# Optimization experiments

Measured on AMD Instinct MI355X. Metric: run time of the kernel, lower is better.

The kernel has to match this reference:

```python
import jax, jax.numpy as jnp
import numpy as np

INF = 100000.0
B, W, T, U, S, N = 64, 16, 64, 128, 20, 8


def setup_inputs() -> dict:
    key = jax.random.key(0)
    ks = jax.random.split(key, 9)
    xavier = (2.0 / (U + U)) ** 0.5
    return {
        "slot_utt_h": jax.random.normal(ks[0], (B, W, T, U), jnp.float32),
        "slot_candidate_c": jax.random.normal(ks[1], (S, U), jnp.float32),
        "status_candidate_c": jax.random.normal(ks[2], (N, U), jnp.float32),
        "position_encoding": jax.random.normal(ks[3], (B, W, S, U), jnp.float32),
        "q_status": jax.random.normal(ks[4], (B, W, N, U), jnp.float32),
        "mask": jnp.zeros((B, W, S * N), jnp.float32),
        "weight": jax.random.normal(ks[5], (U, U), jnp.float32) * xavier,  # bilinear co-attention weight [U,U]
        "W1": jax.random.normal(ks[6], (2 * U, U), jnp.float32) * 0.05,
        "b1": jnp.zeros((U,), jnp.float32),
        "W2": jax.random.normal(ks[7], (U, U), jnp.float32) * 0.05,
        "b2": jnp.zeros((U,), jnp.float32),
        "W3": jax.random.normal(ks[8], (U, 1), jnp.float32) * 0.05,
        "b3": jnp.zeros((1,), jnp.float32),
    }


def _zero_mask(p):
    # original: -(p == 0).float() * INF, added before softmax
    return jnp.where(p == 0.0, -INF, 0.0)


def reference(slot_utt_h, slot_candidate_c, status_candidate_c, position_encoding,
              q_status, mask, weight, W1, b1, W2, b2, W3, b3):
    # ---- attention over utterance tokens ----
    # p[b,w,s,t] = <slot_candidate_c[s], slot_utt_h[b,w,t]>
    p = jnp.einsum('su,bwtu->bwst', slot_candidate_c, slot_utt_h)
    p = jax.nn.softmax(p + _zero_mask(p), axis=-1)
    q_slot = jnp.einsum('bwst,bwtu->bwsu', p, slot_utt_h) + position_encoding  # [B,W,S,U]

    # ---- bilinear co-attention: [B,W*S,U] @ weight @ [B,U,W*N] -> [B,W,S,W,N] ----
    co = jnp.einsum('bwsu,uv,bxnv->bwsxn', q_slot, weight, q_status)
    p2 = jax.nn.softmax(co + _zero_mask(co), axis=3)  # softmax over the second window axis x

    # weighted sum of statuses over window axis x
    q_status_slot = jnp.einsum('bwsxn,bxnu->bwsnu', p2, q_status)  # [B,W,S,N,U]

    q_slot_exp = jnp.broadcast_to(q_slot[:, :, :, None, :], (B, W, S, N, U))
    features = jnp.concatenate([q_slot_exp, q_status_slot], axis=-1)  # [B,W,S,N,2U]

    # ---- MLP (dropout in eval mode = identity) ----
    h = jax.nn.relu(features @ W1 + b1)
    h = jax.nn.relu(h @ W2 + b2)
    logits = h @ W3 + b3  # [B,W,S,N,1]

    logits = logits.reshape(B, W, S * N)
    slot_pred_logits = jnp.max(logits + mask, axis=1)  # masked max-pool over window
    slot_pred_labels = (slot_pred_logits > 0.0).astype(jnp.float32)
    return (slot_pred_labels, S * N, slot_pred_logits)
```

## Files before the change

kernel.cpp:

```cpp
#include <hip/hip_runtime.h>
#include <math.h>

#define INF_ 100000.0f
constexpr int B_ = 64, W_ = 16, T_ = 64, U_ = 128, S_ = 20, N_ = 8;

typedef unsigned short ushort_t;
typedef __attribute__((ext_vector_type(8))) short bf16x8;
typedef __attribute__((ext_vector_type(4))) float floatx4;

static __device__ __forceinline__ unsigned short f2bf(float x) {
    unsigned int u = __float_as_uint(x);
    return (unsigned short)((u + 0x7fff + ((u >> 16) & 1)) >> 16);
}
static __device__ __forceinline__ float bf2f(unsigned short s) {
    return __uint_as_float(((unsigned int)s) << 16);
}

#define HT_SWZ(u, t) ((u) * 72 + ((t) ^ ((((u) >> 3) & 7) << 3)))

__global__ __launch_bounds__(256) void k_pre(
    const float* __restrict__ q_status, const float* __restrict__ weight,
    const float* __restrict__ W1, const float* __restrict__ W2,
    const float* __restrict__ c,
    ushort_t* __restrict__ w1topT, ushort_t* __restrict__ w2T,
    ushort_t* __restrict__ c_bf,
    ushort_t* __restrict__ Gt_bf, ushort_t* __restrict__ qs1T_bf)
{
    __shared__ __align__(16) ushort_t sw[128 * 136];
    __shared__ __align__(16) ushort_t sq[128 * 136];
    const int tid = threadIdx.x, bx = blockIdx.x;

    if (bx < 64) {
        const int b = bx;
        const float* qb = q_status + (size_t)b * 16384;
        for (int i = tid * 4; i < 16384; i += 1024) {
            int r = i >> 7, v = i & 127;
            float4 wv = *(const float4*)&weight[i];
            *(ushort4*)&sw[r * 136 + v] =
                (ushort4){f2bf(wv.x), f2bf(wv.y), f2bf(wv.z), f2bf(wv.w)};
            float4 qv = *(const float4*)&qb[i];
            *(ushort4*)&sq[r * 136 + v] =
                (ushort4){f2bf(qv.x), f2bf(qv.y), f2bf(qv.z), f2bf(qv.w)};
        }
        __syncthreads();
        const int wave = tid >> 6, lane = tid & 63, m16 = lane & 15, q = lane >> 4;
        ushort_t* Gb = Gt_bf + (size_t)b * 16384;
#pragma unroll
        for (int ci = 0; ci < 16; ++ci) {
            int tile = wave * 16 + ci;
            int mt = tile >> 3, jt = tile & 7;
            floatx4 acc = {0.f, 0.f, 0.f, 0.f};
#pragma unroll
            for (int kt = 0; kt < 4; ++kt) {
                bf16x8 a = *(const bf16x8*)&sq[(mt * 16 + m16) * 136 + kt * 32 + q * 8];
                bf16x8 w = *(const bf16x8*)&sw[(jt * 16 + m16) * 136 + kt * 32 + q * 8];
                acc = __builtin_amdgcn_mfma_f32_16x16x32_bf16(a, w, acc, 0, 0, 0);
            }
#pragma unroll
            for (int reg = 0; reg < 4; ++reg)
                Gb[(mt * 16 + q * 4 + reg) * 128 + jt * 16 + m16] = f2bf(acc[reg]);
        }
        return;
    }
    if (bx < 128) {
        const int b = bx - 64;
        const float* qb = q_status + (size_t)b * 16384;
        for (int i = tid * 4; i < 16384; i += 1024) {
            int r = i >> 7, v = i & 127;
            float4 qv = *(const float4*)&qb[i];
            *(ushort4*)&sq[r * 136 + v] =
                (ushort4){f2bf(qv.x), f2bf(qv.y), f2bf(qv.z), f2bf(qv.w)};
            int v2 = i >> 7, j = i & 127;
            float4 wv = *(const float4*)&W1[(128 + v2) * 128 + j];
            sw[(j + 0) * 136 + v2] = f2bf(wv.x);
            sw[(j + 1) * 136 + v2] = f2bf(wv.y);
            sw[(j + 2) * 136 + v2] = f2bf(wv.z);
            sw[(j + 3) * 136 + v2] = f2bf(wv.w);
        }
        __syncthreads();
        const int wave = tid >> 6, lane = tid & 63, m16 = lane & 15, q = lane >> 4;
        ushort_t* Qb = qs1T_bf + (size_t)b * 16384;
#pragma unroll
        for (int ci = 0; ci < 16; ++ci) {
            int tile = wave * 16 + ci;
            int mt = tile >> 3, jt = tile & 7;
            floatx4 acc = {0.f, 0.f, 0.f, 0.f};
#pragma unroll
            for (int kt = 0; kt < 4; ++kt) {
                bf16x8 a = *(const bf16x8*)&sq[(mt * 16 + m16) * 136 + kt * 32 + q * 8];
                bf16x8 w = *(const bf16x8*)&sw[(jt * 16 + m16) * 136 + kt * 32 + q * 8];
                acc = __builtin_amdgcn_mfma_f32_16x16x32_bf16(a, w, acc, 0, 0, 0);
            }
            ushort4 o = {f2bf(acc[0]), f2bf(acc[1]), f2bf(acc[2]), f2bf(acc[3])};
            *(ushort4*)&Qb[(jt * 16 + m16) * 128 + mt * 16 + q * 4] = o;
        }
        return;
    }
    if (bx < 144) {
        int g = (bx - 128) * 1024 + tid * 4;
        int j = g >> 7, k = g & 127;
        *(ushort4*)&w1topT[g] =
            (ushort4){f2bf(W1[k * 128 + j]), f2bf(W1[(k + 1) * 128 + j]),
                      f2bf(W1[(k + 2) * 128 + j]), f2bf(W1[(k + 3) * 128 + j])};
        return;
    }
    if (bx < 160) {
        int g = (bx - 144) * 1024 + tid * 4;
        int j = g >> 7, k = g & 127;
        *(ushort4*)&w2T[g] =
            (ushort4){f2bf(W2[k * 128 + j]), f2bf(W2[(k + 1) * 128 + j]),
                      f2bf(W2[(k + 2) * 128 + j]), f2bf(W2[(k + 3) * 128 + j])};
        return;
    }
    for (int i = tid * 4; i < 4096; i += 1024) {
        int s = i >> 7;
        ushort4 o = {0, 0, 0, 0};
        if (s < 20) {
            float4 v = *(const float4*)&c[i];
            o = (ushort4){f2bf(v.x), f2bf(v.y), f2bf(v.z), f2bf(v.w)};
        }
        *(ushort4*)&c_bf[i] = o;
    }
}

__global__ __launch_bounds__(256) void kA(
    const float* __restrict__ h,
    const ushort_t* __restrict__ c_bf,
    const float* __restrict__ pos,
    ushort_t* __restrict__ q_slot_bf)
{
    __shared__ __align__(16) ushort_t sh_hT[128 * 72];
    __shared__ __align__(16) float    sh_sc[32 * 68];
    __shared__ __align__(16) ushort_t sh_P[32 * 72];

    const int bw = blockIdx.x, tid = threadIdx.x;
    const int wave = tid >> 6, lane = tid & 63, m16 = lane & 15, q = lane >> 4;
    const float* hb = h + (size_t)bw * 8192;

    for (int i = tid * 4; i < 8192; i += 1024) {
        int t = i >> 7, u = i & 127;
        float4 v = *(const float4*)&hb[i];
        sh_hT[HT_SWZ(u + 0, t)] = f2bf(v.x);
        sh_hT[HT_SWZ(u + 1, t)] = f2bf(v.y);
        sh_hT[HT_SWZ(u + 2, t)] = f2bf(v.z);
        sh_hT[HT_SWZ(u + 3, t)] = f2bf(v.w);
    }
    for (int i = tid; i < 2304; i += 256) sh_P[i] = 0;

#pragma unroll
    for (int ci = 0; ci < 2; ++ci) {
        int cmb = wave * 2 + ci;
        int mt = cmb >> 2, jt = cmb & 3;
        floatx4 acc = {0.f, 0.f, 0.f, 0.f};
#pragma unroll
        for (int kt = 0; kt < 4; ++kt) {
            bf16x8 a = *(const bf16x8*)&c_bf[(mt * 16 + m16) * 128 + kt * 32 + q * 8];
            const float* hp = &hb[(jt * 16 + m16) * 128 + kt * 32 + q * 8];
            float4 b0 = *(const float4*)&hp[0];
            float4 b1v = *(const float4*)&hp[4];
            bf16x8 bb;
            bb[0] = (short)f2bf(b0.x); bb[1] = (short)f2bf(b0.y);
            bb[2] = (short)f2bf(b0.z); bb[3] = (short)f2bf(b0.w);
            bb[4] = (short)f2bf(b1v.x); bb[5] = (short)f2bf(b1v.y);
            bb[6] = (short)f2bf(b1v.z); bb[7] = (short)f2bf(b1v.w);
            acc = __builtin_amdgcn_mfma_f32_16x16x32_bf16(a, bb, acc, 0, 0, 0);
        }
#pragma unroll
        for (int reg = 0; reg < 4; ++reg)
            sh_sc[(mt * 16 + q * 4 + reg) * 68 + jt * 16 + m16] = acc[reg];
    }
    __syncthreads();

    for (int s = wave; s < 20; s += 4) {
        float v = sh_sc[s * 68 + lane];
        if (v == 0.0f) v = -INF_;
        float m = v;
        for (int d = 32; d; d >>= 1) m = fmaxf(m, __shfl_xor(m, d));
        float e = expf(v - m);
        float sum = e;
        for (int d = 32; d; d >>= 1) sum += __shfl_xor(sum, d);
        sh_P[s * 72 + lane] = f2bf(e / sum);
    }
    __syncthreads();

    const size_t obase = (size_t)bw * 2560;
#pragma unroll
    for (int ci = 0; ci < 4; ++ci) {
        int cmb = wave * 4 + ci;
        int mt = cmb >> 3, jt = cmb & 7;
        floatx4 acc = {0.f, 0.f, 0.f, 0.f};
#pragma unroll
        for (int kt = 0; kt < 2; ++kt) {
            bf16x8 a = *(const bf16x8*)&sh_P[(mt * 16 + m16) * 72 + kt * 32 + q * 8];
            bf16x8 b = *(const bf16x8*)&sh_hT[HT_SWZ(jt * 16 + m16, kt * 32 + q * 8)];
            acc = __builtin_amdgcn_mfma_f32_16x16x32_bf16(a, b, acc, 0, 0, 0);
        }
        int u = jt * 16 + m16;
#pragma unroll
        for (int reg = 0; reg < 4; ++reg) {
            int row = mt * 16 + q * 4 + reg;
            if (row < 20)
                q_slot_bf[obase + row * 128 + u] =
                    f2bf(acc[reg] + pos[obase + row * 128 + u]);
        }
    }
}

__global__ __launch_bounds__(256) void kB(
    const ushort_t* __restrict__ q_slot_bf,
    const ushort_t* __restrict__ Gt_bf,
    const ushort_t* __restrict__ w1topT,
    const float* __restrict__ b1,
    ushort_t* __restrict__ co_bf,
    float* __restrict__ A)
{
    __shared__ __align__(16) ushort_t shB[128 * 136];
    const int tid = threadIdx.x, bx = blockIdx.x;
    const int wave = tid >> 6, lane = tid & 63, m16 = lane & 15, q = lane >> 4;

    if (bx < 320) {
        const int b = bx / 5, rt = bx - b * 5;
        for (int i = tid * 4; i < 16384; i += 1024)
            *(ushort4*)&shB[(i >> 7) * 136 + (i & 127)] =
                *(const ushort4*)&Gt_bf[(size_t)b * 16384 + i];
        __syncthreads();

        const size_t rbase = (size_t)b * 320 + rt * 64 + wave * 16;
        floatx4 acc[8];
#pragma unroll
        for (int jt = 0; jt < 8; ++jt) acc[jt] = (floatx4){0.f, 0.f, 0.f, 0.f};
#pragma unroll
        for (int kt = 0; kt < 4; ++kt) {
            bf16x8 a = *(const bf16x8*)&q_slot_bf[(rbase + m16) * 128 + kt * 32 + q * 8];
#pragma unroll
            for (int jt = 0; jt < 8; ++jt) {
                bf16x8 g = *(const bf16x8*)&shB[(jt * 16 + m16) * 136 + kt * 32 + q * 8];
                acc[jt] = __builtin_amdgcn_mfma_f32_16x16x32_bf16(a, g, acc[jt], 0, 0, 0);
            }
        }
#pragma unroll
        for (int jt = 0; jt < 8; ++jt)
#pragma unroll
            for (int reg = 0; reg < 4; ++reg)
                co_bf[(rbase + q * 4 + reg) * 128 + jt * 16 + m16] = f2bf(acc[jt][reg]);
    } else {
        const int blk = bx - 320;
        for (int i = tid * 4; i < 16384; i += 1024)
            *(ushort4*)&shB[(i >> 7) * 136 + (i & 127)] =
                *(const ushort4*)&w1topT[i];
        __syncthreads();

        const size_t rbase = (size_t)blk * 64 + wave * 16;
        floatx4 acc[8];
#pragma unroll
        for (int jt = 0; jt < 8; ++jt) acc[jt] = (floatx4){0.f, 0.f, 0.f, 0.f};
#pragma unroll
        for (int kt = 0; kt < 4; ++kt) {
            bf16x8 a = *(const bf16x8*)&q_slot_bf[(rbase + m16) * 128 + kt * 32 + q * 8];
#pragma unroll
            for (int jt = 0; jt < 8; ++jt) {
                bf16x8 g = *(const bf16x8*)&shB[(jt * 16 + m16) * 136 + kt * 32 + q * 8];
                acc[jt] = __builtin_amdgcn_mfma_f32_16x16x32_bf16(a, g, acc[jt], 0, 0, 0);
            }
        }
#pragma unroll
        for (int jt = 0; jt < 8; ++jt) {
            int col = jt * 16 + m16;
            float bv = b1[col];
#pragma unroll
            for (int reg = 0; reg < 4; ++reg)
                A[(rbase + q * 4 + reg) * 128 + col] = acc[jt][reg] + bv;
        }
    }
}

__global__ __launch_bounds__(640, 8) void kC(
    const ushort_t* __restrict__ co_bf,
    const ushort_t* __restrict__ qs1T_bf,
    const float* __restrict__ A,
    const ushort_t* __restrict__ w2T,
    const float* __restrict__ b2,
    const float* __restrict__ W3,
    const float* __restrict__ b3,
    float* __restrict__ lg)
{
    __shared__ __align__(16) ushort_t shB[128 * 136];
    __shared__ __align__(16) ushort_t shP[20 * 132];

    const int bw = blockIdx.x, b = bw >> 4, tid = threadIdx.x;
    const int wave = tid >> 6, lane = tid & 63, m16 = lane & 15, q = lane >> 4;

    for (int i = tid * 4; i < 16384; i += 2560) {
        int r = i >> 7, k = i & 127;
        *(ushort4*)&shB[r * 136 + k] = *(const ushort4*)&qs1T_bf[(size_t)b * 16384 + i];
    }

    {
        int sn = tid >> 2, xi = tid & 3;
        int s = sn >> 3, n2 = sn & 7;
        const ushort_t* crow = co_bf + ((size_t)bw * 20 + s) * 128;
        float v[4];
        float m = -INFINITY;
#pragma unroll
        for (int j = 0; j < 4; ++j) {
            float t = bf2f(crow[(xi + 4 * j) * 8 + n2]);
            if (t == 0.0f) t = -INF_;
            v[j] = t;
            m = fmaxf(m, t);
        }
        m = fmaxf(m, __shfl_xor(m, 1));
        m = fmaxf(m, __shfl_xor(m, 2));
        float sum = 0.f;
#pragma unroll
        for (int j = 0; j < 4; ++j) { v[j] = expf(v[j] - m); sum += v[j]; }
        sum += __shfl_xor(sum, 1);
        sum += __shfl_xor(sum, 2);
        float r = 1.0f / sum;
#pragma unroll
        for (int j = 0; j < 4; ++j)
            shP[s * 132 + (xi + 4 * j) * 8 + n2] = f2bf(v[j] * r);
    }
    __syncthreads();

    const int n = m16 & 7;
    const int sIdx = wave * 2 + (m16 >> 3);

    floatx4 gacc[8];
#pragma unroll
    for (int mt = 0; mt < 8; ++mt) gacc[mt] = (floatx4){0.f, 0.f, 0.f, 0.f};
#pragma unroll
    for (int kt = 0; kt < 4; ++kt) {
        short pv = (short)shP[sIdx * 132 + kt * 32 + q * 8 + n];
        bf16x8 pf = {0, 0, 0, 0, 0, 0, 0, 0};
        pf[0] = (n == 0) ? pv : (short)0;
        pf[1] = (n == 1) ? pv : (short)0;
        pf[2] = (n == 2) ? pv : (short)0;
        pf[3] = (n == 3) ? pv : (short)0;
        pf[4] = (n == 4) ? pv : (short)0;
        pf[5] = (n == 5) ? pv : (short)0;
        pf[6] = (n == 6) ? pv : (short)0;
        pf[7] = (n == 7) ? pv : (short)0;
#pragma unroll
        for (int mt = 0; mt < 8; ++mt) {
            bf16x8 af = *(const bf16x8*)&shB[(mt * 16 + m16) * 136 + kt * 32 + q * 8];
            gacc[mt] = __builtin_amdgcn_mfma_f32_16x16x32_bf16(af, pf, gacc[mt], 0, 0, 0);
        }
    }

    unsigned int h1u[8][2];
    {
        const float* Ab = A + ((size_t)bw * 20 + sIdx) * 128;
#pragma unroll
        for (int mt = 0; mt < 8; ++mt) {
            int u0 = mt * 16 + q * 4;
            float4 av = *(const float4*)&Ab[u0];
            unsigned int x0 = f2bf(fmaxf(gacc[mt][0] + av.x, 0.f));
            unsigned int x1 = f2bf(fmaxf(gacc[mt][1] + av.y, 0.f));
            unsigned int x2 = f2bf(fmaxf(gacc[mt][2] + av.z, 0.f));
            unsigned int x3 = f2bf(fmaxf(gacc[mt][3] + av.w, 0.f));
            h1u[mt][0] = x0 | (x1 << 16);
            h1u[mt][1] = x2 | (x3 << 16);
        }
    }
    __syncthreads();

    for (int i = tid * 4; i < 16384; i += 2560) {
        int r = i >> 7, k = i & 127;
        *(ushort4*)&shB[r * 136 + k] = *(const ushort4*)&w2T[i];
    }
    __syncthreads();

    floatx4 acc[8];
#pragma unroll
    for (int jt = 0; jt < 8; ++jt) acc[jt] = (floatx4){0.f, 0.f, 0.f, 0.f};

    const int sl0 = m16 + 16 * ((2 * q) & 3);
    const int sl1 = m16 + 16 * ((2 * q + 1) & 3);
    const bool hi = (q & 2);
#pragma unroll
    for (int kt = 0; kt < 4; ++kt) {
        int wa0 = __shfl((int)h1u[kt * 2 + 0][0], sl0);
        int wb0 = __shfl((int)h1u[kt * 2 + 1][0], sl0);
        int wa1 = __shfl((int)h1u[kt * 2 + 0][1], sl0);
        int wb1 = __shfl((int)h1u[kt * 2 + 1][1], sl0);
        int wa2 = __shfl((int)h1u[kt * 2 + 0][0], sl1);
        int wb2 = __shfl((int)h1u[kt * 2 + 1][0], sl1);
        int wa3 = __shfl((int)h1u[kt * 2 + 0][1], sl1);
        int wb3 = __shfl((int)h1u[kt * 2 + 1][1], sl1);
        int4 fr;
        fr.x = hi ? wb0 : wa0;
        fr.y = hi ? wb1 : wa1;
        fr.z = hi ? wb2 : wa2;
        fr.w = hi ? wb3 : wa3;
        bf16x8 af2 = *(bf16x8*)&fr;
        const int k0 = kt * 32 + q * 8;
#pragma unroll
        for (int jt = 0; jt < 8; ++jt) {
            bf16x8 bfr = *(const bf16x8*)&shB[(jt * 16 + m16) * 136 + k0];
            acc[jt] = __builtin_amdgcn_mfma_f32_16x16x32_bf16(af2, bfr, acc[jt], 0, 0, 0);
        }
    }

    float b2v[8], w3v[8];
#pragma unroll
    for (int jt = 0; jt < 8; ++jt) {
        b2v[jt] = b2[jt * 16 + m16];
        w3v[jt] = W3[jt * 16 + m16];
    }
    const float b3v = b3[0];
#pragma unroll
    for (int reg = 0; reg < 4; ++reg) {
        float p = 0.f;
#pragma unroll
        for (int jt = 0; jt < 8; ++jt)
            p += fmaxf(acc[jt][reg] + b2v[jt], 0.f) * w3v[jt];
        p += __shfl_xor(p, 1);
        p += __shfl_xor(p, 2);
        p += __shfl_xor(p, 4);
        p += __shfl_xor(p, 8);
        if (m16 == 0)
            lg[(size_t)bw * 160 + wave * 16 + q * 4 + reg] = p + b3v;
    }
}

__global__ __launch_bounds__(256) void k5_final(
    const float* __restrict__ lg,
    const float* __restrict__ mask,
    float* __restrict__ out)
{
    int idx = blockIdx.x * 256 + threadIdx.x;
    const int SN = S_ * N_;
    if (idx < B_ * SN) {
        int b = idx / SN, sn = idx % SN;
        float m = -INFINITY;
        for (int w = 0; w < W_; ++w) {
            float v = lg[((size_t)b * W_ + w) * SN + sn] + mask[((size_t)b * W_ + w) * SN + sn];
            m = fmaxf(m, v);
        }
        out[idx] = (m > 0.f) ? 1.f : 0.f;
        out[B_ * SN + 1 + idx] = m;
    }
    if (idx == 0) out[B_ * SN] = (float)SN;
}

extern "C" void kernel_launch(void* const* d_in, const int* in_sizes, int n_in,
                              void* d_out, int out_size, void* d_ws, size_t ws_size,
                              hipStream_t stream) {
    const float* slot_utt_h = (const float*)d_in[0];
    const float* slot_candidate_c = (const float*)d_in[1];
    const float* position_encoding = (const float*)d_in[3];
    const float* q_status = (const float*)d_in[4];
    const float* mask = (const float*)d_in[5];
    const float* weight = (const float*)d_in[6];
    const float* W1 = (const float*)d_in[7];
    const float* b1 = (const float*)d_in[8];
    const float* W2 = (const float*)d_in[9];
    const float* b2 = (const float*)d_in[10];
    const float* W3 = (const float*)d_in[11];
    const float* b3 = (const float*)d_in[12];
    float* out = (float*)d_out;

    float* f = (float*)d_ws;
    float*    lg        = f + 0;
    float*    A         = f + 163840;
    ushort_t* q_slot_bf = (ushort_t*)(f + 2785280);
    ushort_t* co_bf     = (ushort_t*)(f + 4096000);
    ushort_t* Gt_bf     = (ushort_t*)(f + 5406720);
    ushort_t* qs1T_bf   = (ushort_t*)(f + 5931008);
    ushort_t* w1topT    = (ushort_t*)(f + 6455296);
    ushort_t* w2T       = (ushort_t*)(f + 6463488);
    ushort_t* c_bf      = (ushort_t*)(f + 6471680);

    k_pre<<<161, 256, 0, stream>>>(q_status, weight, W1, W2,
                                   slot_candidate_c,
                                   w1topT, w2T, c_bf, Gt_bf, qs1T_bf);
    kA<<<1024, 256, 0, stream>>>(slot_utt_h, c_bf, position_encoding, q_slot_bf);
    kB<<<640, 256, 0, stream>>>(q_slot_bf, Gt_bf, w1topT, b1, co_bf, A);
    kC<<<1024, 640, 0, stream>>>(co_bf, qs1T_bf, A, w2T, b2, W3, b3, lg);
    k5_final<<<(B_ * S_ * N_ + 255) / 256, 256, 0, stream>>>(lg, mask, out);
}
```

Baseline: 177.3 us.

## Fuse preprocessing with attention kernel and fold co-attention GEMMs into MLP kernel

Merges the weight/status preprocessing kernel and the utterance-attention kernel into one launch, with block ranges selecting the role. The co-attention and W1-top GEMMs formerly in kB are now computed per (b,w) inside the MLP kernel, with results kept in shared memory instead of round-tripping through the co_bf and A global buffers. The c_bf conversion is dropped and candidates are converted inline, and the status GEMMs now read q_status directly from global memory. This removes two launches and global traffic but makes each kCp block do extra small GEMMs reading Gt and w1topT from global memory.

```diff
diff --git a/kernel.cpp b/kernel.cpp
--- a/kernel.cpp
+++ b/kernel.cpp
@@ -18,81 +18,105 @@
 
 #define HT_SWZ(u, t) ((u) * 72 + ((t) ^ ((((u) >> 3) & 7) << 3)))
 
-__global__ __launch_bounds__(256) void k_pre(
+__global__ __launch_bounds__(256) void kAP(
     const float* __restrict__ q_status, const float* __restrict__ weight,
     const float* __restrict__ W1, const float* __restrict__ W2,
     const float* __restrict__ c,
+    const float* __restrict__ h,
+    const float* __restrict__ pos,
     ushort_t* __restrict__ w1topT, ushort_t* __restrict__ w2T,
-    ushort_t* __restrict__ c_bf,
-    ushort_t* __restrict__ Gt_bf, ushort_t* __restrict__ qs1T_bf)
+    ushort_t* __restrict__ Gt_bf, ushort_t* __restrict__ qs1T_bf,
+    ushort_t* __restrict__ q_slot_bf)
 {
-    __shared__ __align__(16) ushort_t sw[128 * 136];
-    __shared__ __align__(16) ushort_t sq[128 * 136];
+    __shared__ __align__(16) ushort_t arena[17408];
     const int tid = threadIdx.x, bx = blockIdx.x;
+    const int wave = tid >> 6, lane = tid & 63, m16 = lane & 15, q = lane >> 4;
+    const bf16x8 zz = {0, 0, 0, 0, 0, 0, 0, 0};
 
     if (bx < 64) {
         const int b = bx;
-        const float* qb = q_status + (size_t)b * 16384;
         for (int i = tid * 4; i < 16384; i += 1024) {
             int r = i >> 7, v = i & 127;
             float4 wv = *(const float4*)&weight[i];
-            *(ushort4*)&sw[r * 136 + v] =
+            *(ushort4*)&arena[r * 136 + v] =
                 (ushort4){f2bf(wv.x), f2bf(wv.y), f2bf(wv.z), f2bf(wv.w)};
-            float4 qv = *(const float4*)&qb[i];
-            *(ushort4*)&sq[r * 136 + v] =
-                (ushort4){f2bf(qv.x), f2bf(qv.y), f2bf(qv.z), f2bf(qv.w)};
         }
         __syncthreads();
-        const int wave = tid >> 6, lane = tid & 63, m16 = lane & 15, q = lane >> 4;
+        const float* qb = q_status + (size_t)b * 16384;
         ushort_t* Gb = Gt_bf + (size_t)b * 16384;
 #pragma unroll
-        for (int ci = 0; ci < 16; ++ci) {
-            int tile = wave * 16 + ci;
-            int mt = tile >> 3, jt = tile & 7;
-            floatx4 acc = {0.f, 0.f, 0.f, 0.f};
+        for (int mt2 = 0; mt2 < 2; ++mt2) {
+            int mt = wave * 2 + mt2;
+            int arow = mt * 16 + m16;
+            bf16x8 afr[4];
 #pragma unroll
             for (int kt = 0; kt < 4; ++kt) {
-                bf16x8 a = *(const bf16x8*)&sq[(mt * 16 + m16) * 136 + kt * 32 + q * 8];
-                bf16x8 w = *(const bf16x8*)&sw[(jt * 16 + m16) * 136 + kt * 32 + q * 8];
-                acc = __builtin_amdgcn_mfma_f32_16x16x32_bf16(a, w, acc, 0, 0, 0);
-            }
-#pragma unroll
-            for (int reg = 0; reg < 4; ++reg)
-                Gb[(mt * 16 + q * 4 + reg) * 128 + jt * 16 + m16] = f2bf(acc[reg]);
+                const float* qp = &qb[arow * 128 + kt * 32 + q * 8];
+                float4 c0 = *(const float4*)&qp[0];
+                float4 c1 = *(const float4*)&qp[4];
+                bf16x8 a;
+                a[0] = (short)f2bf(c0.x); a[1] = (short)f2bf(c0.y);
+                a[2] = (short)f2bf(c0.z); a[3] = (short)f2bf(c0.w);
+                a[4] = (short)f2bf(c1.x); a[5] = (short)f2bf(c1.y);
+                a[6] = (short)f2bf(c1.z); a[7] = (short)f2bf(c1.w);
+                afr[kt] = a;
+            }
+#pragma unroll
+            for (int jt = 0; jt < 8; ++jt) {
+                floatx4 acc = {0.f, 0.f, 0.f, 0.f};
+#pragma unroll
+                for (int kt = 0; kt < 4; ++kt) {
+                    bf16x8 w = *(const bf16x8*)&arena[(jt * 16 + m16) * 136 + kt * 32 + q * 8];
+                    acc = __builtin_amdgcn_mfma_f32_16x16x32_bf16(afr[kt], w, acc, 0, 0, 0);
+                }
+#pragma unroll
+                for (int reg = 0; reg < 4; ++reg)
+                    Gb[(mt * 16 + q * 4 + reg) * 128 + jt * 16 + m16] = f2bf(acc[reg]);
+            }
         }
         return;
     }
     if (bx < 128) {
         const int b = bx - 64;
-        const float* qb = q_status + (size_t)b * 16384;
         for (int i = tid * 4; i < 16384; i += 1024) {
-            int r = i >> 7, v = i & 127;
-            float4 qv = *(const float4*)&qb[i];
-            *(ushort4*)&sq[r * 136 + v] =
-                (ushort4){f2bf(qv.x), f2bf(qv.y), f2bf(qv.z), f2bf(qv.w)};
             int v2 = i >> 7, j = i & 127;
             float4 wv = *(const float4*)&W1[(128 + v2) * 128 + j];
-            sw[(j + 0) * 136 + v2] = f2bf(wv.x);
-            sw[(j + 1) * 136 + v2] = f2bf(wv.y);
-            sw[(j + 2) * 136 + v2] = f2bf(wv.z);
-            sw[(j + 3) * 136 + v2] = f2bf(wv.w);
+            arena[(j + 0) * 136 + v2] = f2bf(wv.x);
+            arena[(j + 1) * 136 + v2] = f2bf(wv.y);
+            arena[(j + 2) * 136 + v2] = f2bf(wv.z);
+            arena[(j + 3) * 136 + v2] = f2bf(wv.w);
         }
         __syncthreads();
-        const int wave = tid >> 6, lane = tid & 63, m16 = lane & 15, q = lane >> 4;
+        const float* qb = q_status + (size_t)b * 16384;
         ushort_t* Qb = qs1T_bf + (size_t)b * 16384;
 #pragma unroll
-        for (int ci = 0; ci < 16; ++ci) {
-            int tile = wave * 16 + ci;
-            int mt = tile >> 3, jt = tile & 7;
-            floatx4 acc = {0.f, 0.f, 0.f, 0.f};
+        for (int mt2 = 0; mt2 < 2; ++mt2) {
+            int mt = wave * 2 + mt2;
+            int arow = mt * 16 + m16;
+            bf16x8 afr[4];
 #pragma unroll
             for (int kt = 0; kt < 4; ++kt) {
-                bf16x8 a = *(const bf16x8*)&sq[(mt * 16 + m16) * 136 + kt * 32 + q * 8];
-                bf16x8 w = *(const bf16x8*)&sw[(jt * 16 + m16) * 136 + kt * 32 + q * 8];
-                acc = __builtin_amdgcn_mfma_f32_16x16x32_bf16(a, w, acc, 0, 0, 0);
-            }
-            ushort4 o = {f2bf(acc[0]), f2bf(acc[1]), f2bf(acc[2]), f2bf(acc[3])};
-            *(ushort4*)&Qb[(jt * 16 + m16) * 128 + mt * 16 + q * 4] = o;
+                const float* qp = &qb[arow * 128 + kt * 32 + q * 8];
+                float4 c0 = *(const float4*)&qp[0];
+                float4 c1 = *(const float4*)&qp[4];
+                bf16x8 a;
+                a[0] = (short)f2bf(c0.x); a[1] = (short)f2bf(c0.y);
+                a[2] = (short)f2bf(c0.z); a[3] = (short)f2bf(c0.w);
+                a[4] = (short)f2bf(c1.x); a[5] = (short)f2bf(c1.y);
+                a[6] = (short)f2bf(c1.z); a[7] = (short)f2bf(c1.w);
+                afr[kt] = a;
+            }
+#pragma unroll
+            for (int jt = 0; jt < 8; ++jt) {
+                floatx4 acc = {0.f, 0.f, 0.f, 0.f};
+#pragma unroll
+                for (int kt = 0; kt < 4; ++kt) {
+                    bf16x8 w = *(const bf16x8*)&arena[(jt * 16 + m16) * 136 + kt * 32 + q * 8];
+                    acc = __builtin_amdgcn_mfma_f32_16x16x32_bf16(afr[kt], w, acc, 0, 0, 0);
+                }
+                ushort4 o = {f2bf(acc[0]), f2bf(acc[1]), f2bf(acc[2]), f2bf(acc[3])};
+                *(ushort4*)&Qb[(jt * 16 + m16) * 128 + mt * 16 + q * 4] = o;
+            }
         }
         return;
     }
@@ -112,29 +136,12 @@
                       f2bf(W2[(k + 2) * 128 + j]), f2bf(W2[(k + 3) * 128 + j])};
         return;
     }
-    for (int i = tid * 4; i < 4096; i += 1024) {
-        int s = i >> 7;
-        ushort4 o = {0, 0, 0, 0};
-        if (s < 20) {
-            float4 v = *(const float4*)&c[i];
-            o = (ushort4){f2bf(v.x), f2bf(v.y), f2bf(v.z), f2bf(v.w)};
-        }
-        *(ushort4*)&c_bf[i] = o;
-    }
-}
-
-__global__ __launch_bounds__(256) void kA(
-    const float* __restrict__ h,
-    const ushort_t* __restrict__ c_bf,
-    const float* __restrict__ pos,
-    ushort_t* __restrict__ q_slot_bf)
-{
-    __shared__ __align__(16) ushort_t sh_hT[128 * 72];
-    __shared__ __align__(16) float    sh_sc[32 * 68];
-    __shared__ __align__(16) ushort_t sh_P[32 * 72];
-
-    const int bw = blockIdx.x, tid = threadIdx.x;
-    const int wave = tid >> 6, lane = tid & 63, m16 = lane & 15, q = lane >> 4;
+
+    ushort_t* sh_hT = arena;
+    float*    sh_sc = (float*)(arena + 9216);
+    ushort_t* sh_P  = arena + 13568;
+
+    const int bw = bx - 160;
     const float* hb = h + (size_t)bw * 8192;
 
     for (int i = tid * 4; i < 8192; i += 1024) {
@@ -151,10 +158,20 @@
     for (int ci = 0; ci < 2; ++ci) {
         int cmb = wave * 2 + ci;
         int mt = cmb >> 2, jt = cmb & 3;
+        int arow = mt * 16 + m16;
         floatx4 acc = {0.f, 0.f, 0.f, 0.f};
 #pragma unroll
         for (int kt = 0; kt < 4; ++kt) {
-            bf16x8 a = *(const bf16x8*)&c_bf[(mt * 16 + m16) * 128 + kt * 32 + q * 8];
+            bf16x8 a = zz;
+            if (arow < 20) {
+                const float* cp = &c[arow * 128 + kt * 32 + q * 8];
+                float4 c0 = *(const float4*)&cp[0];
+                float4 c1 = *(const float4*)&cp[4];
+                a[0] = (short)f2bf(c0.x); a[1] = (short)f2bf(c0.y);
+                a[2] = (short)f2bf(c0.z); a[3] = (short)f2bf(c0.w);
+                a[4] = (short)f2bf(c1.x); a[5] = (short)f2bf(c1.y);
+                a[6] = (short)f2bf(c1.z); a[7] = (short)f2bf(c1.w);
+            }
             const float* hp = &hb[(jt * 16 + m16) * 128 + kt * 32 + q * 8];
             float4 b0 = *(const float4*)&hp[0];
             float4 b1v = *(const float4*)&hp[4];
@@ -206,99 +223,68 @@
     }
 }
 
-__global__ __launch_bounds__(256) void kB(
+__global__ __launch_bounds__(640, 8) void kCp(
     const ushort_t* __restrict__ q_slot_bf,
     const ushort_t* __restrict__ Gt_bf,
     const ushort_t* __restrict__ w1topT,
     const float* __restrict__ b1,
-    ushort_t* __restrict__ co_bf,
-    float* __restrict__ A)
-{
-    __shared__ __align__(16) ushort_t shB[128 * 136];
-    const int tid = threadIdx.x, bx = blockIdx.x;
-    const int wave = tid >> 6, lane = tid & 63, m16 = lane & 15, q = lane >> 4;
-
-    if (bx < 320) {
-        const int b = bx / 5, rt = bx - b * 5;
-        for (int i = tid * 4; i < 16384; i += 1024)
-            *(ushort4*)&shB[(i >> 7) * 136 + (i & 127)] =
-                *(const ushort4*)&Gt_bf[(size_t)b * 16384 + i];
-        __syncthreads();
-
-        const size_t rbase = (size_t)b * 320 + rt * 64 + wave * 16;
-        floatx4 acc[8];
-#pragma unroll
-        for (int jt = 0; jt < 8; ++jt) acc[jt] = (floatx4){0.f, 0.f, 0.f, 0.f};
-#pragma unroll
-        for (int kt = 0; kt < 4; ++kt) {
-            bf16x8 a = *(const bf16x8*)&q_slot_bf[(rbase + m16) * 128 + kt * 32 + q * 8];
-#pragma unroll
-            for (int jt = 0; jt < 8; ++jt) {
-                bf16x8 g = *(const bf16x8*)&shB[(jt * 16 + m16) * 136 + kt * 32 + q * 8];
-                acc[jt] = __builtin_amdgcn_mfma_f32_16x16x32_bf16(a, g, acc[jt], 0, 0, 0);
-            }
-        }
-#pragma unroll
-        for (int jt = 0; jt < 8; ++jt)
-#pragma unroll
-            for (int reg = 0; reg < 4; ++reg)
-                co_bf[(rbase + q * 4 + reg) * 128 + jt * 16 + m16] = f2bf(acc[jt][reg]);
-    } else {
-        const int blk = bx - 320;
-        for (int i = tid * 4; i < 16384; i += 1024)
-            *(ushort4*)&shB[(i >> 7) * 136 + (i & 127)] =
-                *(const ushort4*)&w1topT[i];
-        __syncthreads();
-
-        const size_t rbase = (size_t)blk * 64 + wave * 16;
-        floatx4 acc[8];
-#pragma unroll
-        for (int jt = 0; jt < 8; ++jt) acc[jt] = (floatx4){0.f, 0.f, 0.f, 0.f};
-#pragma unroll
-        for (int kt = 0; kt < 4; ++kt) {
-            bf16x8 a = *(const bf16x8*)&q_slot_bf[(rbase + m16) * 128 + kt * 32 + q * 8];
-#pragma unroll
-            for (int jt = 0; jt < 8; ++jt) {
-                bf16x8 g = *(const bf16x8*)&shB[(jt * 16 + m16) * 136 + kt * 32 + q * 8];
-                acc[jt] = __builtin_amdgcn_mfma_f32_16x16x32_bf16(a, g, acc[jt], 0, 0, 0);
-            }
-        }
-#pragma unroll
-        for (int jt = 0; jt < 8; ++jt) {
-            int col = jt * 16 + m16;
-            float bv = b1[col];
-#pragma unroll
-            for (int reg = 0; reg < 4; ++reg)
-                A[(rbase + q * 4 + reg) * 128 + col] = acc[jt][reg] + bv;
-        }
-    }
-}
-
-__global__ __launch_bounds__(640, 8) void kC(
-    const ushort_t* __restrict__ co_bf,
     const ushort_t* __restrict__ qs1T_bf,
-    const float* __restrict__ A,
     const ushort_t* __restrict__ w2T,
     const float* __restrict__ b2,
     const float* __restrict__ W3,
     const float* __restrict__ b3,
     float* __restrict__ lg)
 {
-    __shared__ __align__(16) ushort_t shB[128 * 136];
-    __shared__ __align__(16) ushort_t shP[20 * 132];
+    __shared__ __align__(16) ushort_t arena[25328];
+    float* Af = (float*)(arena + 20048);
 
     const int bw = blockIdx.x, b = bw >> 4, tid = threadIdx.x;
     const int wave = tid >> 6, lane = tid & 63, m16 = lane & 15, q = lane >> 4;
+    const bf16x8 zz = {0, 0, 0, 0, 0, 0, 0, 0};
 
     for (int i = tid * 4; i < 16384; i += 2560) {
         int r = i >> 7, k = i & 127;
-        *(ushort4*)&shB[r * 136 + k] = *(const ushort4*)&qs1T_bf[(size_t)b * 16384 + i];
-    }
+        *(ushort4*)&arena[r * 136 + k] = *(const ushort4*)&qs1T_bf[(size_t)b * 16384 + i];
+    }
+    {
+        const ushort_t* qsl = q_slot_bf + (size_t)bw * 2560;
+        const ushort_t* Gb = Gt_bf + (size_t)b * 16384;
+        for (int t = wave; t < 32; t += 10) {
+            int isA = t >> 4, tt = t & 15;
+            int mt = tt >> 3, jt = tt & 7;
+            int arow = mt * 16 + m16;
+            const ushort_t* Bsrc = isA ? w1topT : Gb;
+            floatx4 acc = {0.f, 0.f, 0.f, 0.f};
+#pragma unroll
+            for (int kt = 0; kt < 4; ++kt) {
+                bf16x8 a = (arow < 20)
+                    ? *(const bf16x8*)&qsl[arow * 128 + kt * 32 + q * 8] : zz;
+                bf16x8 g = *(const bf16x8*)&Bsrc[(jt * 16 + m16) * 128 + kt * 32 + q * 8];
+                acc = __builtin_amdgcn_mfma_f32_16x16x32_bf16(a, g, acc, 0, 0, 0);
+            }
+            int col = jt * 16 + m16;
+            if (isA) {
+                float bv = b1[col];
+#pragma unroll
+                for (int reg = 0; reg < 4; ++reg) {
+                    int row = mt * 16 + q * 4 + reg;
+                    if (row < 20) Af[row * 132 + col] = acc[reg] + bv;
+                }
+            } else {
+#pragma unroll
+                for (int reg = 0; reg < 4; ++reg) {
+                    int row = mt * 16 + q * 4 + reg;
+                    if (row < 20) arena[17408 + row * 132 + col] = f2bf(acc[reg]);
+                }
+            }
+        }
+    }
+    __syncthreads();
 
     {
         int sn = tid >> 2, xi = tid & 3;
         int s = sn >> 3, n2 = sn & 7;
-        const ushort_t* crow = co_bf + ((size_t)bw * 20 + s) * 128;
+        const ushort_t* crow = &arena[17408 + s * 132];
         float v[4];
         float m = -INFINITY;
 #pragma unroll
@@ -316,9 +302,10 @@
         sum += __shfl_xor(sum, 1);
         sum += __shfl_xor(sum, 2);
         float r = 1.0f / sum;
+        __syncthreads();
 #pragma unroll
         for (int j = 0; j < 4; ++j)
-            shP[s * 132 + (xi + 4 * j) * 8 + n2] = f2bf(v[j] * r);
+            arena[17408 + s * 132 + (xi + 4 * j) * 8 + n2] = f2bf(v[j] * r);
     }
     __syncthreads();
 
@@ -330,7 +317,7 @@
     for (int mt = 0; mt < 8; ++mt) gacc[mt] = (floatx4){0.f, 0.f, 0.f, 0.f};
 #pragma unroll
     for (int kt = 0; kt < 4; ++kt) {
-        short pv = (short)shP[sIdx * 132 + kt * 32 + q * 8 + n];
+        short pv = (short)arena[17408 + sIdx * 132 + kt * 32 + q * 8 + n];
         bf16x8 pf = {0, 0, 0, 0, 0, 0, 0, 0};
         pf[0] = (n == 0) ? pv : (short)0;
         pf[1] = (n == 1) ? pv : (short)0;
@@ -342,14 +329,14 @@
         pf[7] = (n == 7) ? pv : (short)0;
 #pragma unroll
         for (int mt = 0; mt < 8; ++mt) {
-            bf16x8 af = *(const bf16x8*)&shB[(mt * 16 + m16) * 136 + kt * 32 + q * 8];
+            bf16x8 af = *(const bf16x8*)&arena[(mt * 16 + m16) * 136 + kt * 32 + q * 8];
             gacc[mt] = __builtin_amdgcn_mfma_f32_16x16x32_bf16(af, pf, gacc[mt], 0, 0, 0);
         }
     }
 
     unsigned int h1u[8][2];
     {
-        const float* Ab = A + ((size_t)bw * 20 + sIdx) * 128;
+        const float* Ab = Af + sIdx * 132;
 #pragma unroll
         for (int mt = 0; mt < 8; ++mt) {
             int u0 = mt * 16 + q * 4;
@@ -366,7 +353,7 @@
 
     for (int i = tid * 4; i < 16384; i += 2560) {
         int r = i >> 7, k = i & 127;
-        *(ushort4*)&shB[r * 136 + k] = *(const ushort4*)&w2T[i];
+        *(ushort4*)&arena[r * 136 + k] = *(const ushort4*)&w2T[i];
     }
     __syncthreads();
 
@@ -396,7 +383,7 @@
         const int k0 = kt * 32 + q * 8;
 #pragma unroll
         for (int jt = 0; jt < 8; ++jt) {
-            bf16x8 bfr = *(const bf16x8*)&shB[(jt * 16 + m16) * 136 + k0];
+            bf16x8 bfr = *(const bf16x8*)&arena[(jt * 16 + m16) * 136 + k0];
             acc[jt] = __builtin_amdgcn_mfma_f32_16x16x32_bf16(af2, bfr, acc[jt], 0, 0, 0);
         }
     }
@@ -462,20 +449,17 @@
 
     float* f = (float*)d_ws;
     float*    lg        = f + 0;
-    float*    A         = f + 163840;
-    ushort_t* q_slot_bf = (ushort_t*)(f + 2785280);
-    ushort_t* co_bf     = (ushort_t*)(f + 4096000);
-    ushort_t* Gt_bf     = (ushort_t*)(f + 5406720);
-    ushort_t* qs1T_bf   = (ushort_t*)(f + 5931008);
-    ushort_t* w1topT    = (ushort_t*)(f + 6455296);
-    ushort_t* w2T       = (ushort_t*)(f + 6463488);
-    ushort_t* c_bf      = (ushort_t*)(f + 6471680);
-
-    k_pre<<<161, 256, 0, stream>>>(q_status, weight, W1, W2,
-                                   slot_candidate_c,
-                                   w1topT, w2T, c_bf, Gt_bf, qs1T_bf);
-    kA<<<1024, 256, 0, stream>>>(slot_utt_h, c_bf, position_encoding, q_slot_bf);
-    kB<<<640, 256, 0, stream>>>(q_slot_bf, Gt_bf, w1topT, b1, co_bf, A);
-    kC<<<1024, 640, 0, stream>>>(co_bf, qs1T_bf, A, w2T, b2, W3, b3, lg);
+    ushort_t* q_slot_bf = (ushort_t*)(f + 163840);
+    ushort_t* Gt_bf     = (ushort_t*)(f + 1474560);
+    ushort_t* qs1T_bf   = (ushort_t*)(f + 1998848);
+    ushort_t* w1topT    = (ushort_t*)(f + 2523136);
+    ushort_t* w2T       = (ushort_t*)(f + 2531328);
+
+    kAP<<<1184, 256, 0, stream>>>(q_status, weight, W1, W2,
+                                  slot_candidate_c, slot_utt_h,
+                                  position_encoding,
+                                  w1topT, w2T, Gt_bf, qs1T_bf, q_slot_bf);
+    kCp<<<1024, 640, 0, stream>>>(q_slot_bf, Gt_bf, w1topT, b1, qs1T_bf,
+                                  w2T, b2, W3, b3, lg);
     k5_final<<<(B_ * S_ * N_ + 255) / 256, 256, 0, stream>>>(lg, mask, out);
 }
```

Result: slower. 186.2 us (+5.0%).
